# Optimization experiments

Measured on AMD Instinct MI355X. Metric: run time of the kernel, lower is better.

The kernel has to match this reference:

```python
import jax, jax.numpy as jnp
import numpy as np
from jax.ops import segment_sum, segment_max

N_NODES = 50000
N_EDGES = 1600000
IN_DIM = 128
OUT_DIM = 128
N_HEADS = 4
NEG_SLOPE = 0.2

def _leaky(v):
    return jnp.where(v >= 0, v, NEG_SLOPE * v)

def setup_inputs() -> dict:
    key = jax.random.key(0)
    ks = jax.random.split(key, 6)
    x = jax.random.normal(ks[0], (N_NODES, IN_DIM), dtype=jnp.float32)
    edge_index = jax.random.randint(ks[1], (2, N_EDGES), 0, N_NODES, dtype=jnp.int32)
    # xavier-ish small init
    Wq = jax.random.normal(ks[2], (N_HEADS, IN_DIM), dtype=jnp.float32) * 0.1
    Wk = jax.random.normal(ks[3], (N_HEADS, IN_DIM), dtype=jnp.float32) * 0.1
    Wl = jax.random.normal(ks[4], (OUT_DIM, IN_DIM), dtype=jnp.float32) * 0.05
    bl = jax.random.normal(ks[5], (OUT_DIM,), dtype=jnp.float32) * 0.05
    return {"x": x, "edge_index": edge_index, "Wq": Wq, "Wk": Wk, "Wl": Wl, "bl": bl}

def reference(x, edge_index, Wq, Wk, Wl, bl):
    num_nodes = x.shape[0]
    row, col = edge_index[0], edge_index[1]
    # per-head scalar q/k projections, all heads at once: [N, H]
    h_q = x @ Wq.T
    # q_aggregated[i] = sum over edges (i<-j) of h_q[j]
    q_agg = segment_sum(h_q[col], row, num_segments=num_nodes)  # [N, H]
    k_act = _leaky(x @ Wk.T)                                     # [N, H]
    # attention scores per edge per head (head_dim = 1 -> scale 1)
    scores = k_act[row] * q_agg[col]                             # [E, H]
    # segment softmax over incoming edges of each target node (row)
    mx = segment_max(scores, row, num_segments=num_nodes)[row]
    ex = jnp.exp(scores - mx)
    sm = segment_sum(ex, row, num_segments=num_nodes)[row]
    alpha = ex / (sm + 1e-8)                                     # [E, H]
    # values come from the shared W_l projection for every head, so the
    # mean over heads of per-head aggregates equals aggregating with
    # the head-averaged alpha (linearity of segment_sum).
    alpha_mean = alpha.mean(axis=1)                              # [E]
    h_proj = x @ Wl.T + bl                                       # [N, out]
    weighted = alpha_mean[:, None] * h_proj[col]                 # [E, out]
    h_prime = segment_sum(weighted, row, num_segments=num_nodes)  # [N, out]
    return _leaky(h_prime)
```

## Files before the change

### kernel.cpp

```cpp
#include <hip/hip_runtime.h>
#include <cstdint>
#include <cstddef>

typedef unsigned short u16;
typedef unsigned int   u32;
typedef long long      i64;

#define N_NODES 50000
#define N_EDGES 1600000
#define DIM     128
#define NHEADS  4
#define NEG_SLOPE 0.2f
#define CAP     64
#define NB      782
#define SB      512
#define EPB     (N_EDGES / SB)

typedef __attribute__((ext_vector_type(8))) short bf16x8;
typedef __attribute__((ext_vector_type(4))) float f32x4;

__device__ __forceinline__ float b2f(u16 u) {
    union { u32 u; float f; } v; v.u = ((u32)u) << 16; return v.f;
}
__device__ __forceinline__ float bflo(u32 w) {
    union { u32 u; float f; } v; v.u = w << 16; return v.f;
}
__device__ __forceinline__ float bfhi(u32 w) {
    union { u32 u; float f; } v; v.u = w & 0xffff0000u; return v.f;
}
__device__ __forceinline__ u16 f2b(float f) {
    union { float f; u32 u; } v; v.f = f;
    u32 u = v.u;
    u32 r = (u + 0x7fffu + ((u >> 16) & 1u)) >> 16;
    return (u16)r;
}
__device__ __forceinline__ float leaky(float v) {
    return v >= 0.f ? v : NEG_SLOPE * v;
}
__device__ __forceinline__ float fload(const void* p, int f, int idx) {
    return f ? ((const float*)p)[idx] : b2f(((const u16*)p)[idx]);
}
__device__ __forceinline__ int eload(const void* ei, int f64, int idx) {
    return f64 ? (int)((const i64*)ei)[idx] : ((const int*)ei)[idx];
}

__device__ __forceinline__ float bimg_val(
    int row, int col, const void* Wq, const void* Wk, const void* Wl,
    const int* flags)
{
    if (row < 128)      return fload(Wl, flags[3], row * 128 + col);
    if (row < 132)      return fload(Wq, flags[1], (row - 128) * 128 + col);
    if (row < 136)      return fload(Wk, flags[2], (row - 132) * 128 + col);
    if (row < 144)      return 0.f;
    if (row < 148) { const float w = fload(Wq, flags[1], (row - 144) * 128 + col);
                     return w - b2f(f2b(w)); }
    if (row < 152) { const float w = fload(Wk, flags[2], (row - 148) * 128 + col);
                     return w - b2f(f2b(w)); }
    return 0.f;
}

__device__ __forceinline__ int fp32_vote(const u32* p, int K, int lane) {
    int bad = 0;
    for (int i = lane; i < K; i += 64) {
        const u32 w = p[i];
        const u16 lo = (u16)(w & 0xffff);
        const float v = b2f(lo);
        if (lo == 0 || !(fabsf(v) < 1e4f)) ++bad;
    }
    #pragma unroll
    for (int off = 32; off > 0; off >>= 1) bad += __shfl_down(bad, off);
    return bad;
}

__global__ __launch_bounds__(64) void detect_all_kernel(
    const u32* __restrict__ x,  const u32* __restrict__ wq,
    const u32* __restrict__ wk, const u32* __restrict__ wl,
    const u32* __restrict__ bl, const u32* __restrict__ ei,
    int* __restrict__ flags)
{
    const int lane = threadIdx.x;
    int b;
    b = fp32_vote(x,  256, lane); if (lane == 0) flags[0] = (b > 64);
    b = fp32_vote(wq, 128, lane); if (lane == 0) flags[1] = (b > 32);
    b = fp32_vote(wk, 128, lane); if (lane == 0) flags[2] = (b > 32);
    b = fp32_vote(wl, 256, lane); if (lane == 0) flags[3] = (b > 64);
    b = fp32_vote(bl,  64, lane); if (lane == 0) flags[4] = (b > 16);
    int z = 0;
    for (int i = lane; i < 256; i += 64)
        if (ei[2 * i + 1] == 0) ++z;
    #pragma unroll
    for (int off = 32; off > 0; off >>= 1) z += __shfl_down(z, off);
    if (lane == 0) flags[5] = (z > 128);
}

#define W_TOTAL (512 + 512 + 16384 + 128)
#define PACKB_JOBS (160 * 64)
__global__ __launch_bounds__(256) void canon_w_kernel(
    const void* __restrict__ Wq, const void* __restrict__ Wk,
    const void* __restrict__ Wl, const void* __restrict__ bl,
    const int* __restrict__ flags, float* __restrict__ wf,
    u32* __restrict__ wbp)
{
    const int i = blockIdx.x * 256 + threadIdx.x;
    if (i < W_TOTAL) {
        const void* src; int j, f;
        if (i < 512)         { src = Wq; j = i;         f = flags[1]; }
        else if (i < 1024)   { src = Wk; j = i - 512;   f = flags[2]; }
        else if (i < 17408)  { src = Wl; j = i - 1024;  f = flags[3]; }
        else                 { src = bl; j = i - 17408; f = flags[4]; }
        wf[i] = fload(src, f, j);
        return;
    }
    const int w = i - W_TOTAL;
    if (w >= PACKB_JOBS) return;
    const int row  = w >> 6;
    const int col0 = (w & 63) * 2;
    const float v0 = bimg_val(row, col0,     Wq, Wk, Wl, flags);
    const float v1 = bimg_val(row, col0 + 1, Wq, Wk, Wl, flags);
    const int scol0 = col0 ^ ((row & 7) << 3);
    wbp[row * 64 + (scol0 >> 1)] = (u32)f2b(v0) | ((u32)f2b(v1) << 16);
}

__global__ __launch_bounds__(256) void proj_kernel(
    const void* __restrict__ x, const int* __restrict__ flags,
    const float* __restrict__ wf, const u32* __restrict__ wbp,
    u16* __restrict__ h_projb, float* __restrict__ h_q,
    float* __restrict__ k_act)
{
    __shared__ u16 sB[160 * 128];
    const int t  = threadIdx.x;
    const int w  = t >> 6;
    const int l  = t & 63;
    const int lr = l & 15;
    const int lg = l >> 4;
    const int Mb = blockIdx.x * 64 + w * 16;
    const float* bl = wf + 17408;

    u32* sB32 = (u32*)sB;
    #pragma unroll 8
    for (int i = t; i < 160 * 64; i += 256) sB32[i] = wbp[i];
    __syncthreads();

    const int fx = flags[0];
    f32x4 acc[9];
    #pragma unroll
    for (int tt = 0; tt < 8; ++tt) {
        const float bias = bl[tt * 16 + lr];
        acc[tt][0] = bias; acc[tt][1] = bias; acc[tt][2] = bias; acc[tt][3] = bias;
    }
    acc[8][0] = 0.f; acc[8][1] = 0.f; acc[8][2] = 0.f; acc[8][3] = 0.f;

    const int arow = min(Mb + lr, N_NODES - 1);

    #pragma unroll
    for (int kk = 0; kk < 4; ++kk) {
        const int kbase = kk * 32 + lg * 8;
        bf16x8 ahi, alo;
        if (fx == 0) {
            ahi = *(const bf16x8*)((const u16*)x + (size_t)arow * 128 + kbase);
            #pragma unroll
            for (int i = 0; i < 8; ++i) alo[i] = 0;
        } else {
            const float* xf = (const float*)x + (size_t)arow * 128 + kbase;
            const float4 v0 = *(const float4*)xf;
            const float4 v1 = *(const float4*)(xf + 4);
            const float vv[8] = {v0.x, v0.y, v0.z, v0.w, v1.x, v1.y, v1.z, v1.w};
            #pragma unroll
            for (int i = 0; i < 8; ++i) {
                const u16 h = f2b(vv[i]);
                ahi[i] = (short)h;
                alo[i] = (short)f2b(vv[i] - b2f(h));
            }
        }
        #pragma unroll
        for (int tt = 0; tt < 9; ++tt) {
            const int row = tt * 16 + lr;
            const bf16x8 b = *(const bf16x8*)&sB[row * 128 + (kbase ^ ((row & 7) << 3))];
            acc[tt] = __builtin_amdgcn_mfma_f32_16x16x32_bf16(ahi, b, acc[tt], 0, 0, 0);
            if (fx)
                acc[tt] = __builtin_amdgcn_mfma_f32_16x16x32_bf16(alo, b, acc[tt], 0, 0, 0);
        }
        {
            const int row = 144 + lr;
            const bf16x8 b9 = *(const bf16x8*)&sB[row * 128 + (kbase ^ ((row & 7) << 3))];
            acc[8] = __builtin_amdgcn_mfma_f32_16x16x32_bf16(ahi, b9, acc[8], 0, 0, 0);
        }
    }

    #pragma unroll
    for (int tt = 0; tt < 8; ++tt) {
        const int o = tt * 16 + lr;
        #pragma unroll
        for (int j = 0; j < 4; ++j) {
            const int n = Mb + lg * 4 + j;
            if (n < N_NODES) h_projb[(size_t)n * 128 + o] = f2b(acc[tt][j]);
        }
    }
    #pragma unroll
    for (int j = 0; j < 4; ++j) {
        const int n = Mb + lg * 4 + j;
        if (n < N_NODES) {
            if (lr < 4)      h_q[n * 4 + lr] = acc[8][j];
            else if (lr < 8) k_act[n * 4 + (lr - 4)] = leaky(acc[8][j]);
        }
    }
}

__global__ __launch_bounds__(256) void hist_kernel(
    const void* __restrict__ ei, const int* __restrict__ flags,
    u32* __restrict__ rc32, int* __restrict__ hist)
{
    __shared__ int h[NB];
    const int t = threadIdx.x, blk = blockIdx.x;
    for (int i = t; i < NB; i += 256) h[i] = 0;
    __syncthreads();
    const int fe = flags[5];
    const int e0 = blk * EPB;
    const int e1 = min(e0 + EPB, N_EDGES);
    for (int e = e0 + t; e < e1; e += 256) {
        const int r = eload(ei, fe, e);
        const int c = eload(ei, fe, N_EDGES + e);
        rc32[e] = ((u32)r << 16) | (u32)c;
        atomicAdd(&h[r >> 6], 1);
    }
    __syncthreads();
    for (int i = t; i < NB; i += 256) hist[blk * NB + i] = h[i];
}

__device__ __forceinline__ int gperm(int j) {
    return ((j & 63) << 3) | (j >> 6);
}
__global__ __launch_bounds__(256) void scanA_kernel(
    int* __restrict__ hist, int* __restrict__ btot)
{
    __shared__ int part[256];
    const int b = blockIdx.x;
    const int t = threadIdx.x;
    const int b0 = gperm(2 * t), b1 = gperm(2 * t + 1);
    const int v0 = hist[b0 * NB + b];
    const int v1 = hist[b1 * NB + b];
    part[t] = v0 + v1;
    __syncthreads();
    for (int off = 1; off < 256; off <<= 1) {
        const int v = (t >= off) ? part[t - off] : 0;
        __syncthreads();
        part[t] += v;
        __syncthreads();
    }
    const int pre = part[t] - (v0 + v1);
    hist[b0 * NB + b] = pre;
    hist[b1 * NB + b] = pre + v0;
    if (t == 255) btot[b] = part[255];
}

__global__ __launch_bounds__(1024) void scanB_kernel(
    const int* __restrict__ btot, int* __restrict__ btbase)
{
    __shared__ int part[1024];
    const int t = threadIdx.x;
    const int v = (t < NB) ? btot[t] : 0;
    part[t] = v;
    __syncthreads();
    for (int off = 1; off < 1024; off <<= 1) {
        const int x = (t >= off) ? part[t - off] : 0;
        __syncthreads();
        part[t] += x;
        __syncthreads();
    }
    if (t < NB) btbase[t] = part[t] - v;
    if (t == NB - 1) btbase[NB] = part[t];
}

__global__ __launch_bounds__(256) void scatter_kernel(
    const u32* __restrict__ rc32, const int* __restrict__ hist,
    const int* __restrict__ btbase, u32* __restrict__ sorted)
{
    __shared__ int lbase[NB];
    const int t = threadIdx.x, blk = blockIdx.x;
    for (int i = t; i < NB; i += 256)
        lbase[i] = btbase[i] + hist[blk * NB + i];
    __syncthreads();
    const int e0 = blk * EPB;
    const int e1 = min(e0 + EPB, N_EDGES);
    for (int e = e0 + t; e < e1; e += 256) {
        const u32 rc = rc32[e];
        const int p = atomicAdd(&lbase[rc >> 22], 1);
        sorted[p] = rc;
    }
}

__global__ __launch_bounds__(256) void slab_kernel(
    const u32* __restrict__ sorted, const int* __restrict__ btbase,
    int* __restrict__ deg, u16* __restrict__ csr_col,
    int* __restrict__ ovf_cnt, u32* __restrict__ ovf)
{
    __shared__ int cnt[64];
    const int t = threadIdx.x, b = blockIdx.x;
    if (t < 64) cnt[t] = 0;
    __syncthreads();
    const int s0 = btbase[b], s1 = btbase[b + 1];
    for (int i = s0 + t; i < s1; i += 256) {
        const u32 rc = sorted[i];
        const int r = (int)(rc >> 16);
        const int p = atomicAdd(&cnt[r & 63], 1);
        if (p < CAP) csr_col[r * CAP + p] = (u16)(rc & 0xffffu);
        else { const int k = atomicAdd(ovf_cnt, 1); ovf[k] = rc; }
    }
    __syncthreads();
    if (t < 64) {
        const int n = b * 64 + t;
        if (n < N_NODES) deg[n] = cnt[t];
    }
}

__global__ __launch_bounds__(256) void qagg_kernel(
    const int* __restrict__ deg_a, const u16* __restrict__ csr_col,
    const int* __restrict__ ovf_cnt, const u32* __restrict__ ovf,
    const float* __restrict__ h_q, float* __restrict__ q_agg)
{
    const int wave = threadIdx.x >> 6, lane = threadIdx.x & 63;
    const int n = blockIdx.x * 4 + wave;
    if (n >= N_NODES) return;
    const int deg = deg_a[n];
    const int prim = min(deg, CAP);
    float a0 = 0.f, a1 = 0.f, a2 = 0.f, a3 = 0.f;
    if (lane < prim) {
        const int c = csr_col[n * CAP + lane];
        const float4 q = ((const float4*)h_q)[c];
        a0 = q.x; a1 = q.y; a2 = q.z; a3 = q.w;
    }
    if (deg > CAP) {
        const int on = *ovf_cnt;
        for (int i = lane; i < on; i += 64) {
            const u32 pk = ovf[i];
            if ((int)(pk >> 16) == n) {
                const float4 q = ((const float4*)h_q)[pk & 0xffffu];
                a0 += q.x; a1 += q.y; a2 += q.z; a3 += q.w;
            }
        }
    }
    #pragma unroll
    for (int off = 32; off > 0; off >>= 1) {
        a0 += __shfl_down(a0, off); a1 += __shfl_down(a1, off);
        a2 += __shfl_down(a2, off); a3 += __shfl_down(a3, off);
    }
    if (lane == 0) ((float4*)q_agg)[n] = make_float4(a0, a1, a2, a3);
}

__global__ __launch_bounds__(256) void attn_kernel(
    const int* __restrict__ deg_a, const u16* __restrict__ csr_col,
    const int* __restrict__ ovf_cnt, const u32* __restrict__ ovf,
    const float* __restrict__ k_act, const float* __restrict__ q_agg,
    const u16* __restrict__ h_projb, float* __restrict__ out)
{
    const int wave = threadIdx.x >> 6, lane = threadIdx.x & 63;
    const int n = blockIdx.x * 4 + wave;
    if (n >= N_NODES) return;
    const int deg = deg_a[n];
    const int prim = min(deg, CAP);
    const float4 k4 = ((const float4*)k_act)[n];

    int cA = 0;
    float sA0 = -1e30f, sA1 = -1e30f, sA2 = -1e30f, sA3 = -1e30f;
    if (lane < prim) {
        cA = csr_col[n * CAP + lane];
        const float4 q = ((const float4*)q_agg)[cA];
        sA0 = k4.x * q.x; sA1 = k4.y * q.y;
        sA2 = k4.z * q.z; sA3 = k4.w * q.w;
    }
    float m0 = sA0, m1 = sA1, m2 = sA2, m3 = sA3;
    const int ovf_n = (deg > CAP) ? *ovf_cnt : 0;
    for (int i = lane; i < ovf_n; i += 64) {
        const u32 pk = ovf[i];
        if ((int)(pk >> 16) != n) continue;
        const float4 q = ((const float4*)q_agg)[pk & 0xffffu];
        m0 = fmaxf(m0, k4.x * q.x); m1 = fmaxf(m1, k4.y * q.y);
        m2 = fmaxf(m2, k4.z * q.z); m3 = fmaxf(m3, k4.w * q.w);
    }
    #pragma unroll
    for (int off = 32; off > 0; off >>= 1) {
        m0 = fmaxf(m0, __shfl_xor(m0, off));
        m1 = fmaxf(m1, __shfl_xor(m1, off));
        m2 = fmaxf(m2, __shfl_xor(m2, off));
        m3 = fmaxf(m3, __shfl_xor(m3, off));
    }
    const float e0 = __expf(sA0 - m0), e1 = __expf(sA1 - m1);
    const float e2 = __expf(sA2 - m2), e3 = __expf(sA3 - m3);
    float u0 = e0, u1 = e1, u2 = e2, u3 = e3;
    for (int i = lane; i < ovf_n; i += 64) {
        const u32 pk = ovf[i];
        if ((int)(pk >> 16) != n) continue;
        const float4 q = ((const float4*)q_agg)[pk & 0xffffu];
        u0 += __expf(k4.x * q.x - m0); u1 += __expf(k4.y * q.y - m1);
        u2 += __expf(k4.z * q.z - m2); u3 += __expf(k4.w * q.w - m3);
    }
    #pragma unroll
    for (int off = 32; off > 0; off >>= 1) {
        u0 += __shfl_xor(u0, off); u1 += __shfl_xor(u1, off);
        u2 += __shfl_xor(u2, off); u3 += __shfl_xor(u3, off);
    }
    const float r0 = 0.25f / (u0 + 1e-8f), r1 = 0.25f / (u1 + 1e-8f);
    const float r2 = 0.25f / (u2 + 1e-8f), r3 = 0.25f / (u3 + 1e-8f);
    const float a_s = e0 * r0 + e1 * r1 + e2 * r2 + e3 * r3;

    const int sub4 = lane & 15;
    const int eh4  = lane >> 4;
    float acc[8] = {0.f, 0.f, 0.f, 0.f, 0.f, 0.f, 0.f, 0.f};
    const uint4* hp4 = (const uint4*)h_projb;

    #pragma unroll 4
    for (int j = 0; j < prim; j += 4) {
        const int   c = __shfl(cA,  j + eh4);
        const float a = __shfl(a_s, j + eh4);
        const uint4 w = hp4[(size_t)c * 16 + sub4];
        acc[0] = fmaf(a, bflo(w.x), acc[0]);
        acc[1] = fmaf(a, bfhi(w.x), acc[1]);
        acc[2] = fmaf(a, bflo(w.y), acc[2]);
        acc[3] = fmaf(a, bfhi(w.y), acc[3]);
        acc[4] = fmaf(a, bflo(w.z), acc[4]);
        acc[5] = fmaf(a, bfhi(w.z), acc[5]);
        acc[6] = fmaf(a, bflo(w.w), acc[6]);
        acc[7] = fmaf(a, bfhi(w.w), acc[7]);
    }
    for (int base = 0; base < ovf_n; base += 64) {
        const int i = base + lane;
        int   c_s = 0;
        float a_v = 0.f;
        if (i < ovf_n) {
            const u32 pk = ovf[i];
            if ((int)(pk >> 16) == n) {
                c_s = (int)(pk & 0xffffu);
                const float4 q = ((const float4*)q_agg)[c_s];
                a_v = __expf(k4.x * q.x - m0) * r0 + __expf(k4.y * q.y - m1) * r1
                    + __expf(k4.z * q.z - m2) * r2 + __expf(k4.w * q.w - m3) * r3;
            }
        }
        const int cnt = min(64, ovf_n - base);
        for (int j = 0; j < cnt; j += 4) {
            const int   jj = j + eh4;
            const int   c = __shfl(c_s, jj);
            const float a = __shfl(a_v, jj);
            const uint4 w = hp4[(size_t)c * 16 + sub4];
            acc[0] = fmaf(a, bflo(w.x), acc[0]);
            acc[1] = fmaf(a, bfhi(w.x), acc[1]);
            acc[2] = fmaf(a, bflo(w.y), acc[2]);
            acc[3] = fmaf(a, bfhi(w.y), acc[3]);
            acc[4] = fmaf(a, bflo(w.z), acc[4]);
            acc[5] = fmaf(a, bfhi(w.z), acc[5]);
            acc[6] = fmaf(a, bflo(w.w), acc[6]);
            acc[7] = fmaf(a, bfhi(w.w), acc[7]);
        }
    }
    #pragma unroll
    for (int d = 0; d < 8; ++d) {
        acc[d] += __shfl_down(acc[d], 32);
        acc[d] += __shfl_down(acc[d], 16);
    }
    if (eh4 == 0) {
        ((float4*)out)[(size_t)n * 32 + sub4 * 2] =
            make_float4(leaky(acc[0]), leaky(acc[1]), leaky(acc[2]), leaky(acc[3]));
        ((float4*)out)[(size_t)n * 32 + sub4 * 2 + 1] =
            make_float4(leaky(acc[4]), leaky(acc[5]), leaky(acc[6]), leaky(acc[7]));
    }
}

extern "C" void kernel_launch(void* const* d_in, const int* in_sizes, int n_in,
                              void* d_out, int out_size, void* d_ws, size_t ws_size,
                              hipStream_t stream)
{
    const void* x  = d_in[0];
    const void* ei = d_in[1];
    const void* Wq = d_in[2];
    const void* Wk = d_in[3];
    const void* Wl = d_in[4];
    const void* bl = d_in[5];
    float* out = (float*)d_out;

    char* ws = (char*)d_ws;
    size_t off = 0;
    auto alloc = [&](size_t bytes) -> size_t {
        off = (off + 255) & ~(size_t)255;
        size_t o = off; off += bytes; return o;
    };
    const size_t o_flag  = alloc(256);
    const size_t o_wf    = alloc((size_t)W_TOTAL * sizeof(float));
    const size_t o_wbp   = alloc((size_t)PACKB_JOBS * sizeof(u32));
    const size_t o_hq    = alloc((size_t)N_NODES * NHEADS * sizeof(float));
    const size_t o_kact  = alloc((size_t)N_NODES * NHEADS * sizeof(float));
    const size_t o_qagg  = alloc((size_t)N_NODES * NHEADS * sizeof(float));
    const size_t o_hproj = alloc((size_t)N_NODES * DIM * sizeof(u16));
    const size_t o_deg   = alloc((size_t)N_NODES * sizeof(int));
    const size_t o_ovfc  = alloc(256);
    const size_t o_csr   = alloc((size_t)N_NODES * CAP * sizeof(u16));
    const size_t o_ovf   = alloc((size_t)N_EDGES * sizeof(u32));
    const size_t o_rc32  = alloc((size_t)N_EDGES * sizeof(u32));
    const size_t o_sort  = alloc((size_t)N_EDGES * sizeof(u32));
    const size_t o_hist  = alloc((size_t)SB * NB * sizeof(int));
    const size_t o_btot  = alloc((size_t)NB * sizeof(int));
    const size_t o_btb   = alloc((size_t)(NB + 1) * sizeof(int));
    (void)ws_size;

    int*   flags   = (int*)(ws + o_flag);
    float* wf      = (float*)(ws + o_wf);
    u32*   wbp     = (u32*)(ws + o_wbp);
    float* h_q     = (float*)(ws + o_hq);
    float* k_act   = (float*)(ws + o_kact);
    float* q_agg   = (float*)(ws + o_qagg);
    u16*   h_projb = (u16*)(ws + o_hproj);
    int*   deg     = (int*)(ws + o_deg);
    int*   ovf_cnt = (int*)(ws + o_ovfc);
    u16*   csr_col = (u16*)(ws + o_csr);
    u32*   ovf     = (u32*)(ws + o_ovf);
    u32*   rc32    = (u32*)(ws + o_rc32);
    u32*   sorted  = (u32*)(ws + o_sort);
    int*   hist    = (int*)(ws + o_hist);
    int*   btot    = (int*)(ws + o_btot);
    int*   btbase  = (int*)(ws + o_btb);

    hipMemsetAsync(ws + o_ovfc, 0, 256, stream);

    detect_all_kernel<<<1, 64, 0, stream>>>(
        (const u32*)x, (const u32*)Wq, (const u32*)Wk, (const u32*)Wl,
        (const u32*)bl, (const u32*)ei, flags);
    canon_w_kernel<<<(W_TOTAL + PACKB_JOBS + 255) / 256, 256, 0, stream>>>(
        Wq, Wk, Wl, bl, flags, wf, wbp);
    proj_kernel<<<(N_NODES + 63) / 64, 256, 0, stream>>>(
        x, flags, wf, wbp, h_projb, h_q, k_act);
    hist_kernel<<<SB, 256, 0, stream>>>(ei, flags, rc32, hist);
    scanA_kernel<<<NB, 256, 0, stream>>>(hist, btot);
    scanB_kernel<<<1, 1024, 0, stream>>>(btot, btbase);
    scatter_kernel<<<SB, 256, 0, stream>>>(rc32, hist, btbase, sorted);
    slab_kernel<<<NB, 256, 0, stream>>>(sorted, btbase, deg, csr_col,
                                        ovf_cnt, ovf);
    qagg_kernel<<<N_NODES / 4, 256, 0, stream>>>(deg, csr_col, ovf_cnt, ovf,
                                                 h_q, q_agg);
    attn_kernel<<<N_NODES / 4, 256, 0, stream>>>(deg, csr_col, ovf_cnt, ovf,
                                                 k_act, q_agg, h_projb, out);
}
```

Before: 219.0 us.

## Fuse q aggregation into slab kernel and flag detection into weight canon

Removes the separate qagg kernel by accumulating h_q[col] into shared-memory per-node sums with LDS atomics while building the CSR slabs. It also folds the dtype-detection kernel and the overflow-counter memset into canon_w_kernel, where every block recomputes the flags locally. This cuts two launches and one pass over the CSR, at the cost of four LDS float atomics per edge and a float summation order that is no longer deterministic.

```diff
diff --git a/kernel.cpp b/kernel.cpp
--- a/kernel.cpp
+++ b/kernel.cpp
@@ -44,21 +44,6 @@
     return f64 ? (int)((const i64*)ei)[idx] : ((const int*)ei)[idx];
 }
 
-__device__ __forceinline__ float bimg_val(
-    int row, int col, const void* Wq, const void* Wk, const void* Wl,
-    const int* flags)
-{
-    if (row < 128)      return fload(Wl, flags[3], row * 128 + col);
-    if (row < 132)      return fload(Wq, flags[1], (row - 128) * 128 + col);
-    if (row < 136)      return fload(Wk, flags[2], (row - 132) * 128 + col);
-    if (row < 144)      return 0.f;
-    if (row < 148) { const float w = fload(Wq, flags[1], (row - 144) * 128 + col);
-                     return w - b2f(f2b(w)); }
-    if (row < 152) { const float w = fload(Wk, flags[2], (row - 148) * 128 + col);
-                     return w - b2f(f2b(w)); }
-    return 0.f;
-}
-
 __device__ __forceinline__ int fp32_vote(const u32* p, int K, int lane) {
     int bad = 0;
     for (int i = lane; i < K; i += 64) {
@@ -72,42 +57,68 @@
     return bad;
 }
 
-__global__ __launch_bounds__(64) void detect_all_kernel(
-    const u32* __restrict__ x,  const u32* __restrict__ wq,
-    const u32* __restrict__ wk, const u32* __restrict__ wl,
-    const u32* __restrict__ bl, const u32* __restrict__ ei,
-    int* __restrict__ flags)
-{
-    const int lane = threadIdx.x;
-    int b;
-    b = fp32_vote(x,  256, lane); if (lane == 0) flags[0] = (b > 64);
-    b = fp32_vote(wq, 128, lane); if (lane == 0) flags[1] = (b > 32);
-    b = fp32_vote(wk, 128, lane); if (lane == 0) flags[2] = (b > 32);
-    b = fp32_vote(wl, 256, lane); if (lane == 0) flags[3] = (b > 64);
-    b = fp32_vote(bl,  64, lane); if (lane == 0) flags[4] = (b > 16);
-    int z = 0;
-    for (int i = lane; i < 256; i += 64)
-        if (ei[2 * i + 1] == 0) ++z;
-    #pragma unroll
-    for (int off = 32; off > 0; off >>= 1) z += __shfl_down(z, off);
-    if (lane == 0) flags[5] = (z > 128);
+__device__ __forceinline__ void compute_flags(
+    const u32* x, const u32* wq, const u32* wk, const u32* wl,
+    const u32* bl, const u32* ei, int* lf)
+{
+    const int t = threadIdx.x;
+    if (t < 64) {
+        const int lane = t;
+        int b;
+        b = fp32_vote(x,  256, lane); if (lane == 0) lf[0] = (b > 64);
+        b = fp32_vote(wq, 128, lane); if (lane == 0) lf[1] = (b > 32);
+        b = fp32_vote(wk, 128, lane); if (lane == 0) lf[2] = (b > 32);
+        b = fp32_vote(wl, 256, lane); if (lane == 0) lf[3] = (b > 64);
+        b = fp32_vote(bl,  64, lane); if (lane == 0) lf[4] = (b > 16);
+        int z = 0;
+        for (int i = lane; i < 256; i += 64)
+            if (ei[2 * i + 1] == 0) ++z;
+        #pragma unroll
+        for (int off = 32; off > 0; off >>= 1) z += __shfl_down(z, off);
+        if (lane == 0) lf[5] = (z > 128);
+    }
+    __syncthreads();
+}
+
+__device__ __forceinline__ float bimg_val(
+    int row, int col, const void* Wq, const void* Wk, const void* Wl,
+    const int* lf)
+{
+    if (row < 128)      return fload(Wl, lf[3], row * 128 + col);
+    if (row < 132)      return fload(Wq, lf[1], (row - 128) * 128 + col);
+    if (row < 136)      return fload(Wk, lf[2], (row - 132) * 128 + col);
+    if (row < 144)      return 0.f;
+    if (row < 148) { const float w = fload(Wq, lf[1], (row - 144) * 128 + col);
+                     return w - b2f(f2b(w)); }
+    if (row < 152) { const float w = fload(Wk, lf[2], (row - 148) * 128 + col);
+                     return w - b2f(f2b(w)); }
+    return 0.f;
 }
 
 #define W_TOTAL (512 + 512 + 16384 + 128)
 #define PACKB_JOBS (160 * 64)
 __global__ __launch_bounds__(256) void canon_w_kernel(
+    const void* __restrict__ x,  const void* __restrict__ ei,
     const void* __restrict__ Wq, const void* __restrict__ Wk,
     const void* __restrict__ Wl, const void* __restrict__ bl,
-    const int* __restrict__ flags, float* __restrict__ wf,
-    u32* __restrict__ wbp)
-{
+    int* __restrict__ flags, int* __restrict__ ovf_cnt,
+    float* __restrict__ wf, u32* __restrict__ wbp)
+{
+    __shared__ int lf[8];
+    compute_flags((const u32*)x, (const u32*)Wq, (const u32*)Wk,
+                  (const u32*)Wl, (const u32*)bl, (const u32*)ei, lf);
     const int i = blockIdx.x * 256 + threadIdx.x;
+    if (blockIdx.x == 0 && threadIdx.x == 0) {
+        #pragma unroll
+        for (int k = 0; k < 6; ++k) flags[k] = lf[k];
+        *ovf_cnt = 0;
+    }
     if (i < W_TOTAL) {
         const void* src; int j, f;
-        if (i < 512)         { src = Wq; j = i;         f = flags[1]; }
-        else if (i < 1024)   { src = Wk; j = i - 512;   f = flags[2]; }
-        else if (i < 17408)  { src = Wl; j = i - 1024;  f = flags[3]; }
-        else                 { src = bl; j = i - 17408; f = flags[4]; }
+        if (i < 512)         { src = Wq; j = i;         f = lf[1]; }
+        else if (i < 1024)   { src = Wk; j = i - 512;   f = lf[2]; }
+        else if (i < 17408)  { src = Wl; j = i - 1024;  f = lf[3]; }
+        else                 { src = bl; j = i - 17408; f = lf[4]; }
         wf[i] = fload(src, f, j);
         return;
     }
@@ -115,8 +126,8 @@
     if (w >= PACKB_JOBS) return;
     const int row  = w >> 6;
     const int col0 = (w & 63) * 2;
-    const float v0 = bimg_val(row, col0,     Wq, Wk, Wl, flags);
-    const float v1 = bimg_val(row, col0 + 1, Wq, Wk, Wl, flags);
+    const float v0 = bimg_val(row, col0,     Wq, Wk, Wl, lf);
+    const float v1 = bimg_val(row, col0 + 1, Wq, Wk, Wl, lf);
     const int scol0 = col0 ^ ((row & 7) << 3);
     wbp[row * 64 + (scol0 >> 1)] = (u32)f2b(v0) | ((u32)f2b(v1) << 16);
 }
@@ -291,60 +302,43 @@
 
 __global__ __launch_bounds__(256) void slab_kernel(
     const u32* __restrict__ sorted, const int* __restrict__ btbase,
+    const float* __restrict__ h_q,
     int* __restrict__ deg, u16* __restrict__ csr_col,
-    int* __restrict__ ovf_cnt, u32* __restrict__ ovf)
-{
-    __shared__ int cnt[64];
+    int* __restrict__ ovf_cnt, u32* __restrict__ ovf,
+    float* __restrict__ q_agg)
+{
+    __shared__ int   cnt[64];
+    __shared__ float qa[64][4];
     const int t = threadIdx.x, b = blockIdx.x;
-    if (t < 64) cnt[t] = 0;
+    if (t < 64) {
+        cnt[t] = 0;
+        qa[t][0] = 0.f; qa[t][1] = 0.f; qa[t][2] = 0.f; qa[t][3] = 0.f;
+    }
     __syncthreads();
     const int s0 = btbase[b], s1 = btbase[b + 1];
     for (int i = s0 + t; i < s1; i += 256) {
         const u32 rc = sorted[i];
-        const int r = (int)(rc >> 16);
-        const int p = atomicAdd(&cnt[r & 63], 1);
-        if (p < CAP) csr_col[r * CAP + p] = (u16)(rc & 0xffffu);
+        const int r  = (int)(rc >> 16);
+        const int c  = (int)(rc & 0xffffu);
+        const int rl = r & 63;
+        const int p = atomicAdd(&cnt[rl], 1);
+        if (p < CAP) csr_col[r * CAP + p] = (u16)c;
         else { const int k = atomicAdd(ovf_cnt, 1); ovf[k] = rc; }
+        const float4 q = ((const float4*)h_q)[c];
+        atomicAdd(&qa[rl][0], q.x);
+        atomicAdd(&qa[rl][1], q.y);
+        atomicAdd(&qa[rl][2], q.z);
+        atomicAdd(&qa[rl][3], q.w);
     }
     __syncthreads();
     if (t < 64) {
         const int n = b * 64 + t;
-        if (n < N_NODES) deg[n] = cnt[t];
-    }
-}
-
-__global__ __launch_bounds__(256) void qagg_kernel(
-    const int* __restrict__ deg_a, const u16* __restrict__ csr_col,
-    const int* __restrict__ ovf_cnt, const u32* __restrict__ ovf,
-    const float* __restrict__ h_q, float* __restrict__ q_agg)
-{
-    const int wave = threadIdx.x >> 6, lane = threadIdx.x & 63;
-    const int n = blockIdx.x * 4 + wave;
-    if (n >= N_NODES) return;
-    const int deg = deg_a[n];
-    const int prim = min(deg, CAP);
-    float a0 = 0.f, a1 = 0.f, a2 = 0.f, a3 = 0.f;
-    if (lane < prim) {
-        const int c = csr_col[n * CAP + lane];
-        const float4 q = ((const float4*)h_q)[c];
-        a0 = q.x; a1 = q.y; a2 = q.z; a3 = q.w;
-    }
-    if (deg > CAP) {
-        const int on = *ovf_cnt;
-        for (int i = lane; i < on; i += 64) {
-            const u32 pk = ovf[i];
-            if ((int)(pk >> 16) == n) {
-                const float4 q = ((const float4*)h_q)[pk & 0xffffu];
-                a0 += q.x; a1 += q.y; a2 += q.z; a3 += q.w;
-            }
-        }
-    }
-    #pragma unroll
-    for (int off = 32; off > 0; off >>= 1) {
-        a0 += __shfl_down(a0, off); a1 += __shfl_down(a1, off);
-        a2 += __shfl_down(a2, off); a3 += __shfl_down(a3, off);
-    }
-    if (lane == 0) ((float4*)q_agg)[n] = make_float4(a0, a1, a2, a3);
+        if (n < N_NODES) {
+            deg[n] = cnt[t];
+            ((float4*)q_agg)[n] =
+                make_float4(qa[t][0], qa[t][1], qa[t][2], qa[t][3]);
+        }
+    }
 }
 
 __global__ __launch_bounds__(256) void attn_kernel(
@@ -517,23 +511,16 @@
     int*   btot    = (int*)(ws + o_btot);
     int*   btbase  = (int*)(ws + o_btb);
 
-    hipMemsetAsync(ws + o_ovfc, 0, 256, stream);
-
-    detect_all_kernel<<<1, 64, 0, stream>>>(
-        (const u32*)x, (const u32*)Wq, (const u32*)Wk, (const u32*)Wl,
-        (const u32*)bl, (const u32*)ei, flags);
     canon_w_kernel<<<(W_TOTAL + PACKB_JOBS + 255) / 256, 256, 0, stream>>>(
-        Wq, Wk, Wl, bl, flags, wf, wbp);
+        x, ei, Wq, Wk, Wl, bl, flags, ovf_cnt, wf, wbp);
     proj_kernel<<<(N_NODES + 63) / 64, 256, 0, stream>>>(
         x, flags, wf, wbp, h_projb, h_q, k_act);
     hist_kernel<<<SB, 256, 0, stream>>>(ei, flags, rc32, hist);
     scanA_kernel<<<NB, 256, 0, stream>>>(hist, btot);
     scanB_kernel<<<1, 1024, 0, stream>>>(btot, btbase);
     scatter_kernel<<<SB, 256, 0, stream>>>(rc32, hist, btbase, sorted);
-    slab_kernel<<<NB, 256, 0, stream>>>(sorted, btbase, deg, csr_col,
-                                        ovf_cnt, ovf);
-    qagg_kernel<<<N_NODES / 4, 256, 0, stream>>>(deg, csr_col, ovf_cnt, ovf,
-                                                 h_q, q_agg);
+    slab_kernel<<<NB, 256, 0, stream>>>(sorted, btbase, h_q, deg, csr_col,
+                                        ovf_cnt, ovf, q_agg);
     attn_kernel<<<N_NODES / 4, 256, 0, stream>>>(deg, csr_col, ovf_cnt, ovf,
                                                  k_act, q_agg, h_projb, out);
 }
```

After: 240.7 us. 1.1x slower.
